# Optimization experiments

Measured on AMD Instinct MI355X. Metric: run time of the kernel, lower is better.

Reference implementation:

```python
import jax, jax.numpy as jnp
import numpy as np

N, D, E, H, O, TOP_K = 16384, 1024, 8, 2048, 1024, 2
LN_EPS = 1e-5


def _layernorm(h, g, b):
    # h: [E, N, F]; g, b: [E, 1, F]
    mu = h.mean(axis=-1, keepdims=True)
    var = ((h - mu) ** 2).mean(axis=-1, keepdims=True)
    return (h - mu) * jax.lax.rsqrt(var + LN_EPS) * g + b


def setup_inputs() -> dict:
    key = jax.random.key(0)
    ks = jax.random.split(key, 16)
    s = lambda fan_in: 1.0 / np.sqrt(fan_in)
    return {
        "x": jax.random.normal(ks[0], (N, D), dtype=jnp.float32),
        "Wg1": jax.random.uniform(ks[1], (D, 2 * E), jnp.float32, -s(D), s(D)),
        "Wg2": jax.random.uniform(ks[2], (2 * E, E), jnp.float32, -s(2 * E), s(2 * E)),
        "W1": jax.random.uniform(ks[3], (E, D, H), jnp.float32, -s(D), s(D)),
        "b1": jax.random.uniform(ks[4], (E, H), jnp.float32, -s(D), s(D)),
        "g1": jnp.ones((E, H), jnp.float32),
        "be1": jnp.zeros((E, H), jnp.float32),
        "W2": jax.random.uniform(ks[5], (E, H, H), jnp.float32, -s(H), s(H)),
        "b2": jax.random.uniform(ks[6], (E, H), jnp.float32, -s(H), s(H)),
        "g2": jnp.ones((E, H), jnp.float32),
        "be2": jnp.zeros((E, H), jnp.float32),
        "W3": jax.random.uniform(ks[7], (E, H, O), jnp.float32, -s(H), s(H)),
        "b3": jax.random.uniform(ks[8], (E, O), jnp.float32, -s(H), s(H)),
    }


def reference(x, Wg1, Wg2, W1, b1, g1, be1, W2, b2, g2, be2, W3, b3):
    # Gate: Linear(no bias) -> tanh -> Linear(no bias) -> softmax -> top-k
    gate_logits = jnp.tanh(x @ Wg1) @ Wg2                      # [N, E]
    gate_w = jax.nn.softmax(gate_logits, axis=-1)
    topk_w, topk_i = jax.lax.top_k(gate_w, TOP_K)              # [N, K]
    topk_w = topk_w / (topk_w.sum(axis=-1, keepdims=True) + 1e-12)
    # Dense combine weights [N, E] (equals sum over k of routed weight)
    n_idx = jnp.arange(x.shape[0])[:, None]
    cw = jnp.zeros(gate_w.shape, dtype=x.dtype).at[n_idx, topk_i].add(topk_w)
    # Expert MLPs run densely on all tokens (same math as masked dispatch;
    # unselected experts get combine weight 0). Dropout is identity (eval).
    h = jnp.einsum("nd,edh->enh", x, W1) + b1[:, None, :]
    h = jax.nn.gelu(_layernorm(h, g1[:, None, :], be1[:, None, :]), approximate=False)
    h = jnp.einsum("enh,ehk->enk", h, W2) + b2[:, None, :]
    h = jax.nn.gelu(_layernorm(h, g2[:, None, :], be2[:, None, :]), approximate=False)
    y = jnp.einsum("enh,eho->eno", h, W3) + b3[:, None, :]    # [E, N, O]
    return jnp.einsum("eno,ne->no", y, cw)                     # [N, O]
```

## Files before the change

kernel.cpp:

```cpp
#include <hip/hip_runtime.h>
#include <math.h>
#include <stdint.h>

#define N_TOK 16384
#define DIM   1024
#define NEXP  8
#define HID   2048
#define OUTD  1024
#define PADTOT 34816

typedef __attribute__((ext_vector_type(8))) short short8;
typedef __attribute__((ext_vector_type(8))) _Float16 f16x8;
typedef __attribute__((ext_vector_type(4))) float f32x4;
typedef __attribute__((ext_vector_type(4))) unsigned short u16x4;

__device__ __forceinline__ unsigned short f2h(float f) {
  return __builtin_bit_cast(unsigned short, (_Float16)f);
}
__device__ __forceinline__ float h2f(unsigned short h) {
  return (float)__builtin_bit_cast(_Float16, h);
}
__device__ __forceinline__ float gelu_exact(float a) {
  return 0.5f * a * (1.0f + erff(a * 0.70710678118654752f));
}

__global__ __launch_bounds__(256) void wg1t_kernel(
    const float* __restrict__ Wg1, float* __restrict__ Wg1t)
{
  const int t = blockIdx.x * 256 + threadIdx.x;
  const int d0 = t >> 4, j = t & 15;
  f32x4 v;
#pragma unroll
  for (int c = 0; c < 4; ++c) v[c] = Wg1[(size_t)(d0 * 4 + c) * 16 + j];
  *(f32x4*)(Wg1t + (size_t)d0 * 64 + j * 4) = v;
}

__global__ __launch_bounds__(256) void gbconv_kernel(
    const float* __restrict__ g1, const float* __restrict__ b1c,
    const float* __restrict__ g2, const float* __restrict__ b2c,
    unsigned short* __restrict__ dst)
{
  const int i = blockIdx.x * 256 + threadIdx.x;
  const int idx = i * 8;
  const int a = idx >> 14, off = idx & 16383;
  const float* src = (a == 0) ? g1 : (a == 1) ? b1c : (a == 2) ? g2 : b2c;
  f32x4 x0 = *(const f32x4*)(src + off);
  f32x4 x1 = *(const f32x4*)(src + off + 4);
  short8 o;
#pragma unroll
  for (int q = 0; q < 4; ++q) { o[q] = (short)f2h(x0[q]); o[q + 4] = (short)f2h(x1[q]); }
  *(short8*)(dst + idx) = o;
}

__global__ __launch_bounds__(256) void gate_kernel(
    const float* __restrict__ x, const float* __restrict__ Wg1t,
    const float* __restrict__ Wg2,
    int* __restrict__ tok_e, float* __restrict__ tok_w)
{
  const int tid = threadIdx.x;
  const int lane = tid & 63, wid = tid >> 6;
  const int j = lane & 15, g4 = lane >> 4;
  for (int tk = 0; tk < 2; ++tk) {
    const int n = blockIdx.x * 8 + wid * 2 + tk;
    const float* xrow = x + (size_t)n * DIM;
    double acc = 0.0;
    for (int it = 0; it < DIM / 16; ++it) {
      f32x4 xq = *(const f32x4*)(xrow + it * 16 + g4 * 4);
      f32x4 wq = *(const f32x4*)(Wg1t + ((size_t)it * 4 + g4) * 64 + j * 4);
#pragma unroll
      for (int c = 0; c < 4; ++c)
        acc += (double)xq[c] * (double)wq[c];
    }
    acc += __shfl_xor(acc, 16);
    acc += __shfl_xor(acc, 32);
    double t = tanh(acc);
    const int e = lane & 7;
    double ge = 0.0;
#pragma unroll
    for (int jj = 0; jj < 16; ++jj) {
      double tj = __shfl(t, jj);
      ge += tj * (double)Wg2[jj * 8 + e];
    }
    double m = ge;
#pragma unroll
    for (int s = 1; s < 8; s <<= 1) m = fmax(m, __shfl_xor(m, s));
    double p = exp(ge - m);
    double ssum = p;
#pragma unroll
    for (int s = 1; s < 8; s <<= 1) ssum += __shfl_xor(ssum, s);
    double wsm = p / ssum;
    unsigned long long key =
        (((unsigned long long)__double_as_longlong(wsm)) & ~7ULL) |
        (unsigned long long)(7 - e);
    unsigned long long k1 = key;
#pragma unroll
    for (int s = 1; s < 8; s <<= 1) { unsigned long long o = __shfl_xor(k1, s); k1 = (o > k1) ? o : k1; }
    int e1 = 7 - (int)(k1 & 7ULL);
    unsigned long long k2 = (e == e1) ? 0ULL : key;
#pragma unroll
    for (int s = 1; s < 8; s <<= 1) { unsigned long long o = __shfl_xor(k2, s); k2 = (o > k2) ? o : k2; }
    int e2 = 7 - (int)(k2 & 7ULL);
    double w1v = __longlong_as_double((long long)(k1 & ~7ULL));
    double w2v = __longlong_as_double((long long)(k2 & ~7ULL));
    double inv = 1.0 / (w1v + w2v + 1e-12);
    if (lane == 0) {
      tok_e[2 * n] = e1; tok_e[2 * n + 1] = e2;
      tok_w[2 * n] = (float)(w1v * inv); tok_w[2 * n + 1] = (float)(w2v * inv);
    }
  }
}

__global__ __launch_bounds__(256) void hist_kernel(
    const int* __restrict__ tok_e, int* __restrict__ cnt)
{
  __shared__ int h[NEXP];
  const int tid = threadIdx.x;
  if (tid < NEXP) h[tid] = 0;
  __syncthreads();
  const int base = blockIdx.x * 512;
  atomicAdd(&h[tok_e[base + tid]], 1);
  atomicAdd(&h[tok_e[base + 256 + tid]], 1);
  __syncthreads();
  if (tid < NEXP) atomicAdd(&cnt[tid], h[tid]);
}

__global__ void offsets_kernel(const int* __restrict__ cnt, int* __restrict__ off,
                               int* __restrict__ cur) {
  if (threadIdx.x == 0) {
    int a = 0;
    for (int e = 0; e < NEXP; ++e) {
      off[e] = a; cur[e] = a;
      a += (cnt[e] + 255) & ~255;
    }
    off[NEXP] = a;
  }
}

__global__ __launch_bounds__(256) void scatter_kernel(
    const int* __restrict__ tok_e, const float* __restrict__ tok_w,
    int* __restrict__ cur, int* __restrict__ rows, float* __restrict__ roww,
    int* __restrict__ pair)
{
  __shared__ int lcnt[NEXP];
  __shared__ int lbase[NEXP];
  const int tid = threadIdx.x;
  if (tid < NEXP) lcnt[tid] = 0;
  __syncthreads();
  const int n = blockIdx.x * 256 + tid;
  const int e0 = tok_e[2 * n], e1 = tok_e[2 * n + 1];
  const int r0 = atomicAdd(&lcnt[e0], 1);
  const int r1 = atomicAdd(&lcnt[e1], 1);
  __syncthreads();
  if (tid < NEXP) lbase[tid] = atomicAdd(&cur[tid], lcnt[tid]);
  __syncthreads();
  const int p0 = lbase[e0] + r0;
  const int p1 = lbase[e1] + r1;
  rows[p0] = n; roww[p0] = tok_w[2 * n];     pair[2 * n]     = p0;
  rows[p1] = n; roww[p1] = tok_w[2 * n + 1]; pair[2 * n + 1] = p1;
}

__global__ __launch_bounds__(256) void convert_x_kernel(
    const float* __restrict__ x, unsigned short* __restrict__ xh)
{
  size_t i = ((size_t)blockIdx.x * 256 + threadIdx.x) * 8;
  f32x4 a = *(const f32x4*)(x + i);
  f32x4 b = *(const f32x4*)(x + i + 4);
  short8 o;
#pragma unroll
  for (int q = 0; q < 4; ++q) { o[q] = (short)f2h(a[q]); o[q + 4] = (short)f2h(b[q]); }
  *(short8*)(xh + i) = o;
}

__global__ __launch_bounds__(256) void wconv_kernel(
    const float* __restrict__ W, unsigned short* __restrict__ Wt,
    const int K, const int N)
{
  __shared__ float t[64][65];
  const int e = blockIdx.z;
  const float* We = W + (size_t)e * K * N;
  unsigned short* Wte = Wt + (size_t)e * K * N;
  const int n0 = blockIdx.x * 64, k0 = blockIdx.y * 64;
  const int tid = threadIdx.x;
  const int rr0 = tid >> 4, c4 = (tid & 15) * 4;
#pragma unroll
  for (int rr = 0; rr < 4; ++rr) {
    const int r = rr * 16 + rr0;
    f32x4 v = *(const f32x4*)(We + (size_t)(k0 + r) * N + n0 + c4);
    t[r][c4 + 0] = v[0]; t[r][c4 + 1] = v[1]; t[r][c4 + 2] = v[2]; t[r][c4 + 3] = v[3];
  }
  __syncthreads();
#pragma unroll
  for (int rr = 0; rr < 4; ++rr) {
    const int nn = rr * 16 + rr0;
    u16x4 o;
#pragma unroll
    for (int q = 0; q < 4; ++q) o[q] = f2h(t[c4 + q][nn]);
    *(u16x4*)(Wte + (size_t)(n0 + nn) * K + k0 + c4) = o;
  }
}


#define STAGEA(SB_, T_) do {                                                  \
  _Pragma("unroll") for (int qm_ = 0; qm_ < 2; ++qm_)                         \
  _Pragma("unroll") for (int i_ = 0; i_ < 2; ++i_)                            \
    __builtin_amdgcn_global_load_lds(                                         \
      (const __attribute__((address_space(1))) void*)(Abase + aoff[qm_][i_] + (size_t)(T_)*64 + kc8), \
      (__attribute__((address_space(3))) void*)(lds + (SB_)*16384 + qm_*4096 + i_*8192 + tid*8), \
      16, 0, 0);                                                              \
} while (0)

#define STAGEB(SB_, T_) do {                                                  \
  _Pragma("unroll") for (int qn_ = 0; qn_ < 2; ++qn_)                         \
  _Pragma("unroll") for (int i_ = 0; i_ < 2; ++i_)                            \
    __builtin_amdgcn_global_load_lds(                                         \
      (const __attribute__((address_space(1))) void*)(Bbase + boff[qn_][i_] + (size_t)(T_)*64 + kc8), \
      (__attribute__((address_space(3))) void*)(lds + 32768 + (SB_)*16384 + qn_*2048 + (i_*2 + (tid >> 8))*4096 + (tid & 255)*8), \
      16, 0, 0);                                                              \
} while (0)

#define LOAD_AF(QM_) do {                                                     \
    _Pragma("unroll") for (int mi = 0; mi < 4; ++mi)                          \
    _Pragma("unroll") for (int kk = 0; kk < 2; ++kk) {                        \
      const int row_ = wm*128 + (QM_)*64 + mi*16 + l15;                       \
      const int ch_ = ((kk*4 + lh) ^ (row_ & 7));                             \
      af[mi][kk] = *(const short8*)(ldsAb + row_*64 + ch_*8);                 \
    }                                                                         \
} while (0)

#define LOAD_BF() do {                                                        \
    _Pragma("unroll") for (int qn = 0; qn < 2; ++qn)                          \
    _Pragma("unroll") for (int ni = 0; ni < 2; ++ni)                          \
    _Pragma("unroll") for (int kk = 0; kk < 2; ++kk) {                        \
      const int row_ = wn*64 + qn*32 + ni*16 + l15;                           \
      const int ch_ = ((kk*4 + lh) ^ (row_ & 7));                             \
      bf[qn][ni][kk] = *(const short8*)(ldsBb + row_*64 + ch_*8);             \
    }                                                                         \
} while (0)

#define MFMA_HALF(QM_) do {                                                   \
    __builtin_amdgcn_s_setprio(1);                                            \
    _Pragma("unroll") for (int kk = 0; kk < 2; ++kk)                          \
    _Pragma("unroll") for (int mi = 0; mi < 4; ++mi)                          \
    _Pragma("unroll") for (int qn = 0; qn < 2; ++qn)                          \
    _Pragma("unroll") for (int ni = 0; ni < 2; ++ni)                          \
      acc[(QM_)*4 + mi][qn*2 + ni] = __builtin_amdgcn_mfma_f32_16x16x32_f16(  \
          __builtin_bit_cast(f16x8, bf[qn][ni][kk]),                          \
          __builtin_bit_cast(f16x8, af[mi][kk]),                              \
          acc[(QM_)*4 + mi][qn*2 + ni], 0, 0, 0);                             \
    __builtin_amdgcn_s_setprio(0);                                            \
} while (0)

#define SYNC_LGKM_BAR() do {                                                  \
  asm volatile("s_waitcnt lgkmcnt(0)" ::: "memory");                          \
  asm volatile("s_barrier" ::: "memory");                                     \
} while (0)
#define PH_END(N_) do {                                                       \
  asm volatile("s_waitcnt vmcnt(" #N_ ") lgkmcnt(0)" ::: "memory");           \
  asm volatile("s_barrier" ::: "memory");                                     \
} while (0)

template<int MODE>
__global__ __launch_bounds__(512, 1) void gemm256_kernel(
    const unsigned short* __restrict__ Abase,
    const unsigned short* __restrict__ Bbase,
    unsigned short* __restrict__ Oh,
    float* __restrict__ Of,
    const float* __restrict__ bias,
    const int* __restrict__ rows,
    const float* __restrict__ roww,
    const int* __restrict__ off,
    const int K, const int N, const int Astride, const int c0, const int lgGX)
{
  const unsigned orig = blockIdx.x, nwg = gridDim.x;
  const unsigned q8 = nwg >> 3, r8 = nwg & 7;
  const unsigned xcd = orig & 7, pos = orig >> 3;
  const unsigned wrk = (xcd < r8 ? xcd * (q8 + 1) : r8 * (q8 + 1) + (xcd - r8) * q8) + pos;
  const int tn = (int)(wrk & ((1u << lgGX) - 1u));
  const int rowbase = c0 + (int)(wrk >> lgGX) * 256;

  const int off8 = off[NEXP];
  if (rowbase >= off8) return;
  int e = 0;
  while (e < NEXP - 1 && rowbase >= off[e + 1]) ++e;

  __shared__ __align__(16) unsigned short lds[65536];

  const int tid = threadIdx.x, lane = tid & 63, wid = tid >> 6;
  const int wm = wid >> 2, wn = wid & 3;
  const int l15 = lane & 15, lh = lane >> 4;
  const int kc8 = ((tid & 7) ^ ((tid >> 3) & 7)) * 8;

  f32x4 acc[8][4] = {};

  size_t aoff[2][2];
#pragma unroll
  for (int qm = 0; qm < 2; ++qm)
#pragma unroll
    for (int i = 0; i < 2; ++i) {
      int grow = rowbase + i * 128 + qm * 64 + (tid >> 3);
      size_t arow = (MODE == 0) ? (size_t)rows[grow] : (size_t)(grow - c0);
      aoff[qm][i] = arow * (size_t)Astride;
    }
  size_t boff[2][2];
#pragma unroll
  for (int qn = 0; qn < 2; ++qn)
#pragma unroll
    for (int i = 0; i < 2; ++i) {
      int rl = i * 64 + (tid >> 3);
      int brow = (rl >> 5) * 64 + qn * 32 + (rl & 31);
      boff[qn][i] = ((size_t)e * N + (size_t)(tn * 256 + brow)) * (size_t)K;
    }

  const int nt = K >> 6;
  STAGEA(0, 0); STAGEB(0, 0); STAGEB(1, 1);
  PH_END(4);

  for (int t = 0; t < nt; ++t) {
    const int b = t & 1;
    const unsigned short* ldsAb = lds + b * 16384;
    const unsigned short* ldsBb = lds + 32768 + b * 16384;
    short8 af[4][2], bf[2][2][2];
    if (t + 1 < nt) STAGEA(b ^ 1, t + 1);
    LOAD_AF(0); LOAD_BF();
    MFMA_HALF(0);
    SYNC_LGKM_BAR();
    if (t + 2 < nt) STAGEB(b, t + 2);
    LOAD_AF(1);
    MFMA_HALF(1);
    if (t + 2 < nt) PH_END(4); else PH_END(0);
  }

  if (MODE == 2) {
#pragma unroll
    for (int mi = 0; mi < 8; ++mi) {
      int g = rowbase + wm * 128 + mi * 16 + l15;
      int token = rows[g];
      float wgt = roww[g];
#pragma unroll
      for (int ni = 0; ni < 4; ++ni) {
        int n = tn * 256 + wn * 64 + ni * 16 + lh * 4;
        f32x4 v = acc[mi][ni];
        f32x4 bv = *(const f32x4*)(bias + (size_t)e * N + n);
#pragma unroll
        for (int qd = 0; qd < 4; ++qd)
          atomicAdd(&Of[(size_t)token * N + n + qd], wgt * (v[qd] + bv[qd]));
      }
    }
    return;
  }

  __syncthreads();
#pragma unroll
  for (int mi = 0; mi < 8; ++mi) {
    const int row = wm * 128 + mi * 16 + l15;
    float wgt = 1.0f;
    if (MODE == 3) wgt = roww[rowbase + row];
#pragma unroll
    for (int ni = 0; ni < 4; ++ni) {
      const int col = wn * 64 + ni * 16 + lh * 4;
      f32x4 v = acc[mi][ni];
      f32x4 bv = *(const f32x4*)(bias + (size_t)e * N + tn * 256 + col);
      u16x4 h;
#pragma unroll
      for (int qd = 0; qd < 4; ++qd) {
        float vv = v[qd] + bv[qd];
        if (MODE == 3) vv *= wgt;
        h[qd] = f2h(vv);
      }
      const int ch = (col >> 3) ^ (row & 7);
      *(u16x4*)(lds + row * 256 + ch * 8 + (col & 7)) = h;
    }
  }
  __syncthreads();
#pragma unroll
  for (int it = 0; it < 16; ++it) {
    const int flat = it * 512 + tid;
    const int row = flat >> 5;
    const int ch = flat & 31;
    const int chs = ch ^ (row & 7);
    short8 v = *(const short8*)(lds + row * 256 + chs * 8);
    const int g = rowbase + row;
    unsigned short* dst = (MODE == 3) ? (Oh + (size_t)g * N)
                                      : (Oh + (size_t)(g - c0) * N);
    *(short8*)(dst + tn * 256 + ch * 8) = v;
  }
}

__global__ __launch_bounds__(256) void ln_gelu_kernel(
    const unsigned short* __restrict__ src, unsigned short* __restrict__ dst,
    const unsigned short* __restrict__ gamh, const unsigned short* __restrict__ beth,
    const int* __restrict__ off, const int c0)
{
  const int wid = threadIdx.x >> 6, lane = threadIdx.x & 63;
  const int g = c0 + blockIdx.x * 4 + wid;
  if (g >= off[NEXP]) return;
  int e = 0;
#pragma unroll
  for (int q = 1; q < NEXP; ++q) if (g >= off[q]) e = q;
  const unsigned short* s0 = src + (size_t)(g - c0) * HID;
  float v[32];
  float s = 0.f, sq = 0.f;
#pragma unroll
  for (int ch = 0; ch < 4; ++ch) {
    short8 hv = *(const short8*)(s0 + ch * 512 + lane * 8);
#pragma unroll
    for (int q = 0; q < 8; ++q) {
      float f = h2f((unsigned short)hv[q]);
      v[ch * 8 + q] = f;
      s += f; sq += f * f;
    }
  }
#pragma unroll
  for (int sh = 32; sh > 0; sh >>= 1) { s += __shfl_xor(s, sh); sq += __shfl_xor(sq, sh); }
  const float mu  = s * (1.0f / HID);
  const float var = sq * (1.0f / HID) - mu * mu;
  const float rstd = rsqrtf(var + 1e-5f);
  const unsigned short* ge_ = gamh + (size_t)e * HID;
  const unsigned short* be_ = beth + (size_t)e * HID;
  unsigned short* d0 = dst + (size_t)(g - c0) * HID;
#pragma unroll
  for (int ch = 0; ch < 4; ++ch) {
    const int base = ch * 512 + lane * 8;
    short8 gh = *(const short8*)(ge_ + base);
    short8 bh = *(const short8*)(be_ + base);
    short8 o;
#pragma unroll
    for (int q = 0; q < 8; ++q) {
      float t = (v[ch * 8 + q] - mu) * rstd * h2f((unsigned short)gh[q])
                + h2f((unsigned short)bh[q]);
      o[q] = (short)f2h(gelu_exact(t));
    }
    *(short8*)(d0 + base) = o;
  }
}

__global__ __launch_bounds__(256) void combine_kernel(
    const unsigned short* __restrict__ Y, const int* __restrict__ pair,
    float* __restrict__ out)
{
  const int n = blockIdx.x;
  const int j = threadIdx.x * 4;
  const int r1 = pair[2 * n], r2 = pair[2 * n + 1];
  u16x4 a = *(const u16x4*)(Y + (size_t)r1 * OUTD + j);
  u16x4 b = *(const u16x4*)(Y + (size_t)r2 * OUTD + j);
  f32x4 o;
#pragma unroll
  for (int qd = 0; qd < 4; ++qd) o[qd] = h2f(a[qd]) + h2f(b[qd]);
  *(f32x4*)(out + (size_t)n * OUTD + j) = o;
}

__global__ void probe_kernel(float* out, float v) {
  if (threadIdx.x == 0 && blockIdx.x == 0) out[0] = v;
}

extern "C" void kernel_launch(void* const* d_in, const int* in_sizes, int n_in,
                              void* d_out, int out_size, void* d_ws, size_t ws_size,
                              hipStream_t stream) {
  (void)in_sizes; (void)n_in;
  const float* x   = (const float*)d_in[0];
  const float* Wg1 = (const float*)d_in[1];
  const float* Wg2 = (const float*)d_in[2];
  const float* W1  = (const float*)d_in[3];
  const float* b1  = (const float*)d_in[4];
  const float* g1  = (const float*)d_in[5];
  const float* be1 = (const float*)d_in[6];
  const float* W2  = (const float*)d_in[7];
  const float* b2  = (const float*)d_in[8];
  const float* g2  = (const float*)d_in[9];
  const float* be2 = (const float*)d_in[10];
  const float* W3  = (const float*)d_in[11];
  const float* b3  = (const float*)d_in[12];
  float* out = (float*)d_out;

  uint8_t* w = (uint8_t*)d_ws;
  auto alloc = [&](size_t bytes) {
    uint8_t* p = w;
    w += (bytes + 255) & ~(size_t)255;
    return p;
  };
  unsigned short* xh   = (unsigned short*)alloc((size_t)N_TOK * DIM * 2);
  unsigned short* Wt1  = (unsigned short*)alloc((size_t)NEXP * DIM * HID * 2);
  unsigned short* Wt2  = (unsigned short*)alloc((size_t)NEXP * HID * HID * 2);
  unsigned short* Wt3  = (unsigned short*)alloc((size_t)NEXP * HID * OUTD * 2);
  float* Wg1t  = (float*)alloc((size_t)DIM * 16 * 4);
  unsigned short* gbh = (unsigned short*)alloc((size_t)4 * NEXP * HID * 2);
  int*   rows  = (int*)alloc((size_t)PADTOT * 4);
  float* roww  = (float*)alloc((size_t)PADTOT * 4);
  int*   tok_e = (int*)alloc((size_t)2 * N_TOK * 4);
  float* tok_w = (float*)alloc((size_t)2 * N_TOK * 4);
  int*   pair  = (int*)alloc((size_t)2 * N_TOK * 4);
  int*   cnt   = (int*)alloc(256);
  int*   off   = (int*)alloc(256);
  int*   cur   = (int*)alloc(256);
  size_t fixed_used = (size_t)(w - (uint8_t*)d_ws);

  long long availLL = (long long)ws_size - (long long)fixed_used - 4096;
  int R = 0;
  if (availLL > 0) {
    long long r = availLL / (HID * 2 + HID * 2);
    if (r > PADTOT) r = PADTOT;
    R = (int)(r & ~255LL);
  }
  if (R < 256) {
    hipMemsetAsync(d_out, 0, (size_t)out_size * sizeof(float), stream);
    probe_kernel<<<1, 64, 0, stream>>>(out, (float)(ws_size >> 20));
    return;
  }
  unsigned short* act1h = (unsigned short*)alloc((size_t)R * HID * 2);
  unsigned short* act2  = (unsigned short*)alloc((size_t)R * HID * 2);
  const bool single = (R >= PADTOT);
  unsigned short* Yh = act1h;

  hipMemsetAsync(cnt, 0, NEXP * sizeof(int), stream);
  hipMemsetAsync(rows, 0, (size_t)PADTOT * 4, stream);
  hipMemsetAsync(roww, 0, (size_t)PADTOT * 4, stream);
  if (!single)
    hipMemsetAsync(d_out, 0, (size_t)out_size * sizeof(float), stream);

  wg1t_kernel<<<16, 256, 0, stream>>>(Wg1, Wg1t);
  gbconv_kernel<<<32, 256, 0, stream>>>(g1, be1, g2, be2, gbh);
  gate_kernel<<<N_TOK / 8, 256, 0, stream>>>(x, Wg1t, Wg2, tok_e, tok_w);
  hist_kernel<<<2 * N_TOK / 512, 256, 0, stream>>>(tok_e, cnt);
  offsets_kernel<<<1, 64, 0, stream>>>(cnt, off, cur);
  scatter_kernel<<<N_TOK / 256, 256, 0, stream>>>(tok_e, tok_w, cur, rows, roww, pair);

  convert_x_kernel<<<(N_TOK * DIM / 8) / 256, 256, 0, stream>>>(x, xh);
  wconv_kernel<<<dim3(HID / 64, DIM / 64, NEXP), 256, 0, stream>>>(W1, Wt1, DIM, HID);
  wconv_kernel<<<dim3(HID / 64, HID / 64, NEXP), 256, 0, stream>>>(W2, Wt2, HID, HID);
  wconv_kernel<<<dim3(OUTD / 64, HID / 64, NEXP), 256, 0, stream>>>(W3, Wt3, HID, OUTD);

  const unsigned short* g1h  = gbh;
  const unsigned short* be1h = gbh + (size_t)NEXP * HID;
  const unsigned short* g2h  = gbh + (size_t)2 * NEXP * HID;
  const unsigned short* be2h = gbh + (size_t)3 * NEXP * HID;

  for (int c0 = 0; c0 < PADTOT; c0 += R) {
    int Rc = PADTOT - c0; if (Rc > R) Rc = R;
    const int yt = Rc / 256;
    gemm256_kernel<0><<<8 * yt, 512, 0, stream>>>(xh, Wt1, act1h, nullptr, b1,
                                                  rows, roww, off, DIM, HID, DIM, c0, 3);
    ln_gelu_kernel<<<Rc / 4, 256, 0, stream>>>(act1h, act2, g1h, be1h, off, c0);
    gemm256_kernel<1><<<8 * yt, 512, 0, stream>>>(act2, Wt2, act1h, nullptr, b2,
                                                  rows, roww, off, HID, HID, HID, c0, 3);
    ln_gelu_kernel<<<Rc / 4, 256, 0, stream>>>(act1h, act2, g2h, be2h, off, c0);
    if (single)
      gemm256_kernel<3><<<4 * yt, 512, 0, stream>>>(act2, Wt3, Yh, nullptr, b3,
                                                    rows, roww, off, HID, OUTD, HID, c0, 2);
    else
      gemm256_kernel<2><<<4 * yt, 512, 0, stream>>>(act2, Wt3, nullptr, out, b3,
                                                    rows, roww, off, HID, OUTD, HID, c0, 2);
  }
  if (single)
    combine_kernel<<<N_TOK, 256, 0, stream>>>(Yh, pair, out);
}
```

Measured before the change: 1.010 ms.

## Switch expert GEMM inner loop to 32x32x16 MFMA tiles

Replaces the 16x16x32 f16 MFMA micro-tiling with 32x32x16 MFMA, restructuring the LDS fragment loads, accumulator layout (f32x16[4][2]) and epilogue indexing to match. The larger MFMA shape cuts the number of LDS fragment reads per FLOP and the instruction count, and the A-fragment loads are now interleaved with MFMAs per 32-row subtile. The cost is different register pressure and a different output lane mapping in the epilogue, which adds risk of layout errors.

```diff
diff --git a/kernel.cpp b/kernel.cpp
--- a/kernel.cpp
+++ b/kernel.cpp
@@ -12,6 +12,7 @@
 typedef __attribute__((ext_vector_type(8))) short short8;
 typedef __attribute__((ext_vector_type(8))) _Float16 f16x8;
 typedef __attribute__((ext_vector_type(4))) float f32x4;
+typedef __attribute__((ext_vector_type(16))) float f32x16;
 typedef __attribute__((ext_vector_type(4))) unsigned short u16x4;
 
 __device__ __forceinline__ unsigned short f2h(float f) {
@@ -218,35 +219,31 @@
       16, 0, 0);                                                              \
 } while (0)
 
-#define LOAD_AF(QM_) do {                                                     \
-    _Pragma("unroll") for (int mi = 0; mi < 4; ++mi)                          \
-    _Pragma("unroll") for (int kk = 0; kk < 2; ++kk) {                        \
-      const int row_ = wm*128 + (QM_)*64 + mi*16 + l15;                       \
-      const int ch_ = ((kk*4 + lh) ^ (row_ & 7));                             \
-      af[mi][kk] = *(const short8*)(ldsAb + row_*64 + ch_*8);                 \
+#define LOAD_AF32(MT_) do {                                                   \
+    _Pragma("unroll") for (int ks = 0; ks < 4; ++ks) {                        \
+      const int row_ = wm*128 + (MT_)*32 + l31;                               \
+      const int ch_ = ((ks*2 + lh5) ^ (row_ & 7));                            \
+      af[ks] = *(const short8*)(ldsAb + row_*64 + ch_*8);                     \
     }                                                                         \
 } while (0)
 
-#define LOAD_BF() do {                                                        \
-    _Pragma("unroll") for (int qn = 0; qn < 2; ++qn)                          \
-    _Pragma("unroll") for (int ni = 0; ni < 2; ++ni)                          \
-    _Pragma("unroll") for (int kk = 0; kk < 2; ++kk) {                        \
-      const int row_ = wn*64 + qn*32 + ni*16 + l15;                           \
-      const int ch_ = ((kk*4 + lh) ^ (row_ & 7));                             \
-      bf[qn][ni][kk] = *(const short8*)(ldsBb + row_*64 + ch_*8);             \
+#define LOAD_BF32() do {                                                      \
+    _Pragma("unroll") for (int ntl = 0; ntl < 2; ++ntl)                       \
+    _Pragma("unroll") for (int ks = 0; ks < 4; ++ks) {                        \
+      const int row_ = wn*64 + ntl*32 + l31;                                  \
+      const int ch_ = ((ks*2 + lh5) ^ (row_ & 7));                            \
+      bf[ntl][ks] = *(const short8*)(ldsBb + row_*64 + ch_*8);                \
     }                                                                         \
 } while (0)
 
-#define MFMA_HALF(QM_) do {                                                   \
+#define MFMA_MT(MT_) do {                                                     \
     __builtin_amdgcn_s_setprio(1);                                            \
-    _Pragma("unroll") for (int kk = 0; kk < 2; ++kk)                          \
-    _Pragma("unroll") for (int mi = 0; mi < 4; ++mi)                          \
-    _Pragma("unroll") for (int qn = 0; qn < 2; ++qn)                          \
-    _Pragma("unroll") for (int ni = 0; ni < 2; ++ni)                          \
-      acc[(QM_)*4 + mi][qn*2 + ni] = __builtin_amdgcn_mfma_f32_16x16x32_f16(  \
-          __builtin_bit_cast(f16x8, bf[qn][ni][kk]),                          \
-          __builtin_bit_cast(f16x8, af[mi][kk]),                              \
-          acc[(QM_)*4 + mi][qn*2 + ni], 0, 0, 0);                             \
+    _Pragma("unroll") for (int ks = 0; ks < 4; ++ks)                          \
+    _Pragma("unroll") for (int ntl = 0; ntl < 2; ++ntl)                       \
+      acc[MT_][ntl] = __builtin_amdgcn_mfma_f32_32x32x16_f16(                 \
+          __builtin_bit_cast(f16x8, bf[ntl][ks]),                             \
+          __builtin_bit_cast(f16x8, af[ks]),                                  \
+          acc[MT_][ntl], 0, 0, 0);                                            \
     __builtin_amdgcn_s_setprio(0);                                            \
 } while (0)
 
@@ -287,10 +284,10 @@
 
   const int tid = threadIdx.x, lane = tid & 63, wid = tid >> 6;
   const int wm = wid >> 2, wn = wid & 3;
-  const int l15 = lane & 15, lh = lane >> 4;
+  const int l31 = lane & 31, lh5 = lane >> 5;
   const int kc8 = ((tid & 7) ^ ((tid >> 3) & 7)) * 8;
 
-  f32x4 acc[8][4] = {};
+  f32x16 acc[4][2] = {};
 
   size_t aoff[2][2];
 #pragma unroll
@@ -319,57 +316,61 @@
     const int b = t & 1;
     const unsigned short* ldsAb = lds + b * 16384;
     const unsigned short* ldsBb = lds + 32768 + b * 16384;
-    short8 af[4][2], bf[2][2][2];
+    short8 af[4], bf[2][4];
     if (t + 1 < nt) STAGEA(b ^ 1, t + 1);
-    LOAD_AF(0); LOAD_BF();
-    MFMA_HALF(0);
+    LOAD_BF32();
+    LOAD_AF32(0); MFMA_MT(0);
+    LOAD_AF32(1); MFMA_MT(1);
     SYNC_LGKM_BAR();
     if (t + 2 < nt) STAGEB(b, t + 2);
-    LOAD_AF(1);
-    MFMA_HALF(1);
+    LOAD_AF32(2); MFMA_MT(2);
+    LOAD_AF32(3); MFMA_MT(3);
     if (t + 2 < nt) PH_END(4); else PH_END(0);
   }
 
   if (MODE == 2) {
 #pragma unroll
-    for (int mi = 0; mi < 8; ++mi) {
-      int g = rowbase + wm * 128 + mi * 16 + l15;
-      int token = rows[g];
-      float wgt = roww[g];
-#pragma unroll
-      for (int ni = 0; ni < 4; ++ni) {
-        int n = tn * 256 + wn * 64 + ni * 16 + lh * 4;
-        f32x4 v = acc[mi][ni];
-        f32x4 bv = *(const f32x4*)(bias + (size_t)e * N + n);
-#pragma unroll
-        for (int qd = 0; qd < 4; ++qd)
-          atomicAdd(&Of[(size_t)token * N + n + qd], wgt * (v[qd] + bv[qd]));
-      }
+    for (int mt = 0; mt < 4; ++mt) {
+      const int grow = rowbase + wm * 128 + mt * 32 + l31;
+      const int token = rows[grow];
+      const float wgt = roww[grow];
+#pragma unroll
+      for (int ntl = 0; ntl < 2; ++ntl)
+#pragma unroll
+        for (int gg = 0; gg < 4; ++gg) {
+          const int n = tn * 256 + wn * 64 + ntl * 32 + gg * 8 + lh5 * 4;
+          f32x4 bv = *(const f32x4*)(bias + (size_t)e * N + n);
+#pragma unroll
+          for (int qd = 0; qd < 4; ++qd)
+            atomicAdd(&Of[(size_t)token * N + n + qd],
+                      wgt * (acc[mt][ntl][gg * 4 + qd] + bv[qd]));
+        }
     }
     return;
   }
 
   __syncthreads();
 #pragma unroll
-  for (int mi = 0; mi < 8; ++mi) {
-    const int row = wm * 128 + mi * 16 + l15;
+  for (int mt = 0; mt < 4; ++mt) {
+    const int row = wm * 128 + mt * 32 + l31;
     float wgt = 1.0f;
     if (MODE == 3) wgt = roww[rowbase + row];
 #pragma unroll
-    for (int ni = 0; ni < 4; ++ni) {
-      const int col = wn * 64 + ni * 16 + lh * 4;
-      f32x4 v = acc[mi][ni];
-      f32x4 bv = *(const f32x4*)(bias + (size_t)e * N + tn * 256 + col);
-      u16x4 h;
-#pragma unroll
-      for (int qd = 0; qd < 4; ++qd) {
-        float vv = v[qd] + bv[qd];
-        if (MODE == 3) vv *= wgt;
-        h[qd] = f2h(vv);
+    for (int ntl = 0; ntl < 2; ++ntl)
+#pragma unroll
+      for (int gg = 0; gg < 4; ++gg) {
+        const int col = wn * 64 + ntl * 32 + gg * 8 + lh5 * 4;
+        f32x4 bv = *(const f32x4*)(bias + (size_t)e * N + tn * 256 + col);
+        u16x4 h;
+#pragma unroll
+        for (int qd = 0; qd < 4; ++qd) {
+          float vv = acc[mt][ntl][gg * 4 + qd] + bv[qd];
+          if (MODE == 3) vv *= wgt;
+          h[qd] = f2h(vv);
+        }
+        const int ch = col >> 3;
+        *(u16x4*)(lds + row * 256 + (ch ^ (row & 7)) * 8 + (col & 7)) = h;
       }
-      const int ch = (col >> 3) ^ (row & 7);
-      *(u16x4*)(lds + row * 256 + ch * 8 + (col & 7)) = h;
-    }
   }
   __syncthreads();
 #pragma unroll
```

Measured after the change: 1.092 ms. 1.08x slower.
